# Optimization experiments

Measured on AMD Instinct MI355X. Metric: run time of the kernel, lower is better.

## Reference

```python
import jax, jax.numpy as jnp
import numpy as np

N_C, N_S, D = 16384, 16384, 2688  # 128x128 hypercolumn grid, VGG16 concat channels
EPS = 1e-8


def setup_inputs() -> dict:
    key = jax.random.key(0)
    k1, k2 = jax.random.split(key)
    feats_c = jax.random.normal(k1, (N_C, D), dtype=jnp.float32)
    feats_s = jax.random.normal(k2, (N_S, D), dtype=jnp.float32)
    return {"feats_c": feats_c, "feats_s": feats_s}


def reference(feats_c, feats_s):
    # NNST replace_features: for each content hypercolumn vector, find the
    # style feature vector with max cosine similarity and take it as target.
    cn = feats_c * jax.lax.rsqrt(jnp.sum(feats_c * feats_c, axis=1, keepdims=True) + EPS)
    sn = feats_s * jax.lax.rsqrt(jnp.sum(feats_s * feats_s, axis=1, keepdims=True) + EPS)
    sim = jnp.einsum("cd,sd->cs", cn, sn)  # [N_C, N_S] cosine similarity
    idx = jnp.argmax(sim, axis=1)           # nearest style feature per content pixel
    target_feats = jnp.take(feats_s, idx, axis=0)  # gather un-normalized style feats
    return target_feats
```

## Files before the change

### kernel.cpp

```cpp
#include <hip/hip_runtime.h>
#include <stdint.h>

typedef unsigned short ushort_t;
typedef unsigned int u32;
typedef unsigned long long u64;

#define NC_ 16384
#define NS_ 16384
#define DIM 2688
#define D4 (DIM / 4)
#define KSTEPS (DIM / 32)

typedef __attribute__((ext_vector_type(8))) short short8;
typedef __attribute__((ext_vector_type(4))) float f32x4;


__device__ inline ushort_t f2bf(float x) {
  u32 u = __float_as_uint(x);
  u32 r = u + 0x7FFFu + ((u >> 16) & 1u);
  return (ushort_t)(r >> 16);
}
__device__ inline float bf2f(ushort_t b) { return __uint_as_float(((u32)b) << 16); }

__device__ inline u32 fkey(float f) {
  u32 u = __float_as_uint(f);
  return (u & 0x80000000u) ? ~u : (u | 0x80000000u);
}

__device__ inline void async16(const void* g, void* l) {
  __builtin_amdgcn_global_load_lds(
      (const __attribute__((address_space(1))) u32*)g,
      (__attribute__((address_space(3))) u32*)l, 16, 0, 0);
}

__device__ inline int swz(int r, int q) {
  return ((r >> 1) << 6) + (((((r & 1) << 2) | q) ^ ((r >> 1) & 7)) << 3);
}


__global__ __launch_bounds__(256) void content_split_kernel(
    const float* __restrict__ fc, ushort_t* __restrict__ c_hi, ushort_t* __restrict__ c_lo) {
  size_t i = (size_t)blockIdx.x * 256 + threadIdx.x;
  if (i >= (size_t)NC_ * DIM / 4) return;
  float4 v = ((const float4*)fc)[i];
  ushort4 h, l;
  h.x = f2bf(v.x); l.x = f2bf(v.x - bf2f(h.x));
  h.y = f2bf(v.y); l.y = f2bf(v.y - bf2f(h.y));
  h.z = f2bf(v.z); l.z = f2bf(v.z - bf2f(h.z));
  h.w = f2bf(v.w); l.w = f2bf(v.w - bf2f(h.w));
  ((ushort4*)c_hi)[i] = h;
  ((ushort4*)c_lo)[i] = l;
}


__global__ __launch_bounds__(256) void style_split_kernel(
    const float* __restrict__ fs, ushort_t* __restrict__ s_hi, ushort_t* __restrict__ s_lo) {
  const int s = blockIdx.x, t = threadIdx.x;
  const float4* row = (const float4*)(fs + (size_t)s * DIM);
  float ss = 0.f;
  for (int i = t; i < D4; i += 256) {
    float4 v = row[i];
    ss += v.x * v.x + v.y * v.y + v.z * v.z + v.w * v.w;
  }
#pragma unroll
  for (int off = 32; off >= 1; off >>= 1) ss += __shfl_xor(ss, off, 64);
  __shared__ float wsum[4];
  if ((t & 63) == 0) wsum[t >> 6] = ss;
  __syncthreads();
  float scale = rsqrtf(wsum[0] + wsum[1] + wsum[2] + wsum[3] + 1e-8f);
  ushort4* h4 = (ushort4*)(s_hi + (size_t)s * DIM);
  ushort4* l4 = (ushort4*)(s_lo + (size_t)s * DIM);
  for (int i = t; i < D4; i += 256) {
    float4 v = row[i];
    float x = v.x * scale, y = v.y * scale, z = v.z * scale, w = v.w * scale;
    ushort4 h, l;
    h.x = f2bf(x); l.x = f2bf(x - bf2f(h.x));
    h.y = f2bf(y); l.y = f2bf(y - bf2f(h.y));
    h.z = f2bf(z); l.z = f2bf(z - bf2f(h.z));
    h.w = f2bf(w); l.w = f2bf(w - bf2f(h.w));
    h4[i] = h;
    l4[i] = l;
  }
}


__global__ __launch_bounds__(256, 2) void sim_argmax_kernel(
    const ushort_t* __restrict__ c_hi, const ushort_t* __restrict__ c_lo,
    const ushort_t* __restrict__ s_hi, const ushort_t* __restrict__ s_lo,
    u64* __restrict__ partial) {
  __shared__ __align__(16) ushort_t lds[24576];
  __shared__ u64 red[128][2];

  ushort_t* la_hi = lds;
  ushort_t* la_lo = lds + 4096;
  ushort_t* lb_hi = lds + 8192;
  ushort_t* lb_lo = lds + 16384;

  const int t = threadIdx.x;
  const int bid = blockIdx.x;
  const int grp = bid >> 8;
  const int wi = bid & 255;
  const int cb = (grp & 7) * 16 + (wi & 15);
  const int sb = (grp >> 3) * 16 + (wi >> 4);

  const ushort_t* gah = c_hi + (size_t)cb * 128 * DIM;
  const ushort_t* gal = c_lo + (size_t)cb * 128 * DIM;
  const ushort_t* gbh = s_hi + (size_t)sb * 256 * DIM;
  const ushort_t* gbl = s_lo + (size_t)sb * 256 * DIM;

  const int lane = t & 63;
  const int wave = t >> 6;
  const int wy = wave >> 1, wx = wave & 1;
  const int lm = lane & 15, q = lane >> 4;

  f32x4 acc[4][8];
#pragma unroll
  for (int i = 0; i < 4; i++)
#pragma unroll
    for (int j = 0; j < 8; j++) acc[i][j] = (f32x4){0.f, 0.f, 0.f, 0.f};

  const int tw = t & 192;

  for (int ks = 0; ks < KSTEPS; ++ks) {
    const int kel = ks * 32;
#pragma unroll
    for (int j = 0; j < 2; ++j) {
      int e = j * 256 + t;
      int rp = e >> 3;
      int cc = (e & 7) ^ (rp & 7);
      int row = (rp << 1) | (cc >> 2);
      size_t goff = (size_t)row * DIM + kel + (cc & 3) * 8;
      int loff = (j * 256 + tw) * 8;
      async16(gah + goff, la_hi + loff);
      async16(gal + goff, la_lo + loff);
    }
#pragma unroll
    for (int j = 0; j < 4; ++j) {
      int e = j * 256 + t;
      int rp = e >> 3;
      int cc = (e & 7) ^ (rp & 7);
      int row = (rp << 1) | (cc >> 2);
      size_t goff = (size_t)row * DIM + kel + (cc & 3) * 8;
      int loff = (j * 256 + tw) * 8;
      async16(gbh + goff, lb_hi + loff);
      async16(gbl + goff, lb_lo + loff);
    }
    __syncthreads();

    short8 ah[4], al[4];
#pragma unroll
    for (int mi = 0; mi < 4; ++mi) {
      int r = swz(wy * 64 + mi * 16 + lm, q);
      ah[mi] = *(const short8*)(la_hi + r);
      al[mi] = *(const short8*)(la_lo + r);
    }
#pragma unroll
    for (int h = 0; h < 2; ++h) {
      short8 bh[4], bl[4];
#pragma unroll
      for (int nj = 0; nj < 4; ++nj) {
        int r = swz(wx * 128 + (h * 4 + nj) * 16 + lm, q);
        bh[nj] = *(const short8*)(lb_hi + r);
        bl[nj] = *(const short8*)(lb_lo + r);
      }
#pragma unroll
      for (int mi = 0; mi < 4; ++mi)
#pragma unroll
        for (int nj = 0; nj < 4; ++nj) {
          int ni = h * 4 + nj;
          acc[mi][ni] = __builtin_amdgcn_mfma_f32_16x16x32_bf16(ah[mi], bh[nj], acc[mi][ni], 0, 0, 0);
          acc[mi][ni] = __builtin_amdgcn_mfma_f32_16x16x32_bf16(ah[mi], bl[nj], acc[mi][ni], 0, 0, 0);
          acc[mi][ni] = __builtin_amdgcn_mfma_f32_16x16x32_bf16(al[mi], bh[nj], acc[mi][ni], 0, 0, 0);
        }
    }
    __syncthreads();
  }

#pragma unroll
  for (int mi = 0; mi < 4; ++mi) {
#pragma unroll
    for (int r = 0; r < 4; ++r) {
      float bv = acc[mi][0][r];
      int bn = 0;
#pragma unroll
      for (int ni = 1; ni < 8; ++ni) {
        float v = acc[mi][ni][r];
        if (v > bv) { bv = v; bn = ni; }
      }
      u32 colg = (u32)(sb * 256 + wx * 128 + bn * 16 + lm);
      u64 key = ((u64)fkey(bv) << 32) | (u64)(0xFFFFFFFFu - colg);
#pragma unroll
      for (int off = 8; off >= 1; off >>= 1) {
        u64 o = __shfl_xor((unsigned long long)key, off, 64);
        if (o > key) key = o;
      }
      if (lm == 0) red[wy * 64 + mi * 16 + q * 4 + r][wx] = key;
    }
  }
  __syncthreads();
  if (t < 128) {
    u64 k0 = red[t][0], k1 = red[t][1];
    u64 b = k0 > k1 ? k0 : k1;
    partial[((size_t)(cb * 128 + t)) * 64 + sb] = b;
  }
}


__global__ __launch_bounds__(256) void argmax_gather_kernel(
    const u64* __restrict__ partial, const float* __restrict__ fs, float* __restrict__ out) {
  const int m = blockIdx.x, t = threadIdx.x;
  __shared__ u64 sbest;
  if (t < 64) {
    u64 key = partial[(size_t)m * 64 + t];
#pragma unroll
    for (int off = 32; off >= 1; off >>= 1) {
      u64 o = __shfl_xor((unsigned long long)key, off, 64);
      if (o > key) key = o;
    }
    if (t == 0) sbest = key;
  }
  __syncthreads();
  u64 best = sbest;
  u32 col = 0xFFFFFFFFu - (u32)best;
  const float4* src = (const float4*)(fs + (size_t)col * DIM);
  float4* dst = (float4*)(out + (size_t)m * DIM);
  for (int i = t; i < D4; i += 256) dst[i] = src[i];
}


extern "C" void kernel_launch(void* const* d_in, const int* in_sizes, int n_in,
                              void* d_out, int out_size, void* d_ws, size_t ws_size,
                              hipStream_t stream) {
  const float* fc = (const float*)d_in[0];
  const float* fs = (const float*)d_in[1];
  float* out = (float*)d_out;

  ushort_t* c_hi = (ushort_t*)d_ws;
  ushort_t* c_lo = c_hi + (size_t)NC_ * DIM;
  ushort_t* s_hi = c_lo + (size_t)NC_ * DIM;
  ushort_t* s_lo = s_hi + (size_t)NS_ * DIM;
  u64* partial = (u64*)(s_lo + (size_t)NS_ * DIM);

  content_split_kernel<<<(NC_ * DIM / 4 + 255) / 256, 256, 0, stream>>>(fc, c_hi, c_lo);
  style_split_kernel<<<NS_, 256, 0, stream>>>(fs, s_hi, s_lo);
  sim_argmax_kernel<<<8192, 256, 0, stream>>>(c_hi, c_lo, s_hi, s_lo, partial);
  argmax_gather_kernel<<<NC_, 256, 0, stream>>>(partial, fs, out);
}
```

Before: 3.815 ms.

## Switch sim GEMM to 32x32x16 MFMA tiles and reuse LDS for reduction

Replaces the 16x16x32 bf16 MFMA tiling with 32x32x16 MFMAs (2x4 tiles of 32x32 per wave), which halves the number of LDS fragment loads per MFMA work and reduces instruction count. The argmax epilogue is remapped to the 32x32 accumulator layout. The reduction scratch now aliases the main LDS buffer, and launch bounds request 3 blocks per SM. The added occupancy target may constrain registers and cause spills, given the 128 accumulator registers.

```diff
diff --git a/kernel.cpp b/kernel.cpp
--- a/kernel.cpp
+++ b/kernel.cpp
@@ -12,7 +12,7 @@
 #define KSTEPS (DIM / 32)
 
 typedef __attribute__((ext_vector_type(8))) short short8;
-typedef __attribute__((ext_vector_type(4))) float f32x4;
+typedef __attribute__((ext_vector_type(16))) float f32x16;
 
 
 __device__ inline ushort_t f2bf(float x) {
@@ -84,17 +84,17 @@
 }
 
 
-__global__ __launch_bounds__(256, 2) void sim_argmax_kernel(
+__global__ __launch_bounds__(256, 3) void sim_argmax_kernel(
     const ushort_t* __restrict__ c_hi, const ushort_t* __restrict__ c_lo,
     const ushort_t* __restrict__ s_hi, const ushort_t* __restrict__ s_lo,
     u64* __restrict__ partial) {
   __shared__ __align__(16) ushort_t lds[24576];
-  __shared__ u64 red[128][2];
 
   ushort_t* la_hi = lds;
   ushort_t* la_lo = lds + 4096;
   ushort_t* lb_hi = lds + 8192;
   ushort_t* lb_lo = lds + 16384;
+  u64 (*red)[2] = (u64(*)[2])lds;
 
   const int t = threadIdx.x;
   const int bid = blockIdx.x;
@@ -111,13 +111,16 @@
   const int lane = t & 63;
   const int wave = t >> 6;
   const int wy = wave >> 1, wx = wave & 1;
-  const int lm = lane & 15, q = lane >> 4;
-
-  f32x4 acc[4][8];
-#pragma unroll
-  for (int i = 0; i < 4; i++)
-#pragma unroll
-    for (int j = 0; j < 8; j++) acc[i][j] = (f32x4){0.f, 0.f, 0.f, 0.f};
+  const int lr = lane & 31;
+  const int kq = lane >> 5;
+
+  f32x16 acc[2][4];
+#pragma unroll
+  for (int i = 0; i < 2; i++)
+#pragma unroll
+    for (int j = 0; j < 4; j++)
+#pragma unroll
+      for (int r = 0; r < 16; r++) acc[i][j][r] = 0.f;
 
   const int tw = t & 192;
 
@@ -147,54 +150,62 @@
     }
     __syncthreads();
 
-    short8 ah[4], al[4];
-#pragma unroll
-    for (int mi = 0; mi < 4; ++mi) {
-      int r = swz(wy * 64 + mi * 16 + lm, q);
-      ah[mi] = *(const short8*)(la_hi + r);
-      al[mi] = *(const short8*)(la_lo + r);
-    }
+    short8 ah[2][2], al[2][2];
+#pragma unroll
+    for (int mi = 0; mi < 2; ++mi)
+#pragma unroll
+      for (int ku = 0; ku < 2; ++ku) {
+        int r = swz(wy * 64 + mi * 32 + lr, ku * 2 + kq);
+        ah[mi][ku] = *(const short8*)(la_hi + r);
+        al[mi][ku] = *(const short8*)(la_lo + r);
+      }
 #pragma unroll
     for (int h = 0; h < 2; ++h) {
-      short8 bh[4], bl[4];
-#pragma unroll
-      for (int nj = 0; nj < 4; ++nj) {
-        int r = swz(wx * 128 + (h * 4 + nj) * 16 + lm, q);
-        bh[nj] = *(const short8*)(lb_hi + r);
-        bl[nj] = *(const short8*)(lb_lo + r);
-      }
-#pragma unroll
-      for (int mi = 0; mi < 4; ++mi)
-#pragma unroll
-        for (int nj = 0; nj < 4; ++nj) {
-          int ni = h * 4 + nj;
-          acc[mi][ni] = __builtin_amdgcn_mfma_f32_16x16x32_bf16(ah[mi], bh[nj], acc[mi][ni], 0, 0, 0);
-          acc[mi][ni] = __builtin_amdgcn_mfma_f32_16x16x32_bf16(ah[mi], bl[nj], acc[mi][ni], 0, 0, 0);
-          acc[mi][ni] = __builtin_amdgcn_mfma_f32_16x16x32_bf16(al[mi], bh[nj], acc[mi][ni], 0, 0, 0);
+      short8 bh[2][2], bl[2][2];
+#pragma unroll
+      for (int nj = 0; nj < 2; ++nj)
+#pragma unroll
+        for (int ku = 0; ku < 2; ++ku) {
+          int r = swz(wx * 128 + (h * 2 + nj) * 32 + lr, ku * 2 + kq);
+          bh[nj][ku] = *(const short8*)(lb_hi + r);
+          bl[nj][ku] = *(const short8*)(lb_lo + r);
         }
+#pragma unroll
+      for (int mi = 0; mi < 2; ++mi)
+#pragma unroll
+        for (int nj = 0; nj < 2; ++nj) {
+          int ni = h * 2 + nj;
+#pragma unroll
+          for (int ku = 0; ku < 2; ++ku) {
+            acc[mi][ni] = __builtin_amdgcn_mfma_f32_32x32x16_bf16(ah[mi][ku], bh[nj][ku], acc[mi][ni], 0, 0, 0);
+            acc[mi][ni] = __builtin_amdgcn_mfma_f32_32x32x16_bf16(ah[mi][ku], bl[nj][ku], acc[mi][ni], 0, 0, 0);
+            acc[mi][ni] = __builtin_amdgcn_mfma_f32_32x32x16_bf16(al[mi][ku], bh[nj][ku], acc[mi][ni], 0, 0, 0);
+          }
+        }
     }
     __syncthreads();
   }
 
 #pragma unroll
-  for (int mi = 0; mi < 4; ++mi) {
-#pragma unroll
-    for (int r = 0; r < 4; ++r) {
+  for (int mi = 0; mi < 2; ++mi) {
+#pragma unroll
+    for (int r = 0; r < 16; ++r) {
       float bv = acc[mi][0][r];
       int bn = 0;
 #pragma unroll
-      for (int ni = 1; ni < 8; ++ni) {
+      for (int ni = 1; ni < 4; ++ni) {
         float v = acc[mi][ni][r];
         if (v > bv) { bv = v; bn = ni; }
       }
-      u32 colg = (u32)(sb * 256 + wx * 128 + bn * 16 + lm);
+      u32 colg = (u32)(sb * 256 + wx * 128 + bn * 32 + lr);
       u64 key = ((u64)fkey(bv) << 32) | (u64)(0xFFFFFFFFu - colg);
 #pragma unroll
-      for (int off = 8; off >= 1; off >>= 1) {
+      for (int off = 16; off >= 1; off >>= 1) {
         u64 o = __shfl_xor((unsigned long long)key, off, 64);
         if (o > key) key = o;
       }
-      if (lm == 0) red[wy * 64 + mi * 16 + q * 4 + r][wx] = key;
+      int row_local = wy * 64 + mi * 32 + (r & 3) + 8 * (r >> 2) + 4 * kq;
+      if (lr == 0) red[row_local][wx] = key;
     }
   }
   __syncthreads();
```

Measured after the change: 5.058 ms. 32.6% more time.
